# Kernel optimization log

Hardware: AMD Instinct MI355X
Metric: run time of the kernel (lower is better)

The kernel has to match this reference:

```python
import jax, jax.numpy as jnp
import numpy as np

N, E, A, S = 100000, 1600000, 500000, 50000
F_IN, W, LAYERS = 64, 64, 3


def setup_inputs() -> dict:
    key = jax.random.key(0)
    ks = jax.random.split(key, 20)

    def glorot(k, shape):
        fan_in = shape[-2]
        return jax.random.normal(k, shape, dtype=jnp.float32) / jnp.sqrt(jnp.float32(fan_in))

    return {
        "x": jax.random.normal(ks[0], (N, F_IN), dtype=jnp.float32),
        "edge_src": jax.random.randint(ks[1], (E,), 0, N, dtype=jnp.int32),
        "edge_dst": jax.random.randint(ks[2], (E,), 0, N, dtype=jnp.int32),
        "gather_idx": jax.random.randint(ks[3], (A,), 0, N, dtype=jnp.int32),
        "seg_idx": jax.random.randint(ks[4], (A,), 0, S, dtype=jnp.int32),
        # GraphConv 0: lin_root (no bias) + lin_rel (bias)
        "w_root0": glorot(ks[5], (F_IN, W)),
        "w_rel0": glorot(ks[6], (F_IN, W)),
        "b0": jnp.zeros((W,), jnp.float32),
        # hidden GraphConv layers, stacked
        "w_root_h": glorot(ks[7], (LAYERS - 1, W, W)),
        "w_rel_h": glorot(ks[8], (LAYERS - 1, W, W)),
        "b_h": jnp.zeros((LAYERS - 1, W), jnp.float32),
        # MLP head
        "fc1_w": glorot(ks[9], (W, W)),
        "fc1_b": jnp.zeros((W,), jnp.float32),
        "fc2_w": glorot(ks[10], (W, 32)),
        "fc2_b": jnp.zeros((32,), jnp.float32),
        "fc3_w": glorot(ks[11], (32, 2)),
        "fc3_b": jnp.zeros((2,), jnp.float32),
        "num_sets": S,
    }


def _graph_conv(h, edge_src, edge_dst, w_root, w_rel, b):
    # PyG GraphConv (aggr='add'): out_i = W_root h_i + W_rel * sum_{j->i} h_j + b
    agg = jax.ops.segment_sum(h[edge_src], edge_dst, num_segments=h.shape[0])
    return h @ w_root + agg @ w_rel + b


def reference(x, edge_src, edge_dst, gather_idx, seg_idx,
              w_root0, w_rel0, b0, w_root_h, w_rel_h, b_h,
              fc1_w, fc1_b, fc2_w, fc2_b, fc3_w, fc3_b, num_sets):
    h = jax.nn.elu(_graph_conv(x, edge_src, edge_dst, w_root0, w_rel0, b0))
    for i in range(w_root_h.shape[0]):
        h = jax.nn.elu(_graph_conv(h, edge_src, edge_dst, w_root_h[i], w_rel_h[i], b_h[i]))
    # set pooling: gather node rows then scatter_add into sets
    pooled = jax.ops.segment_sum(h[gather_idx], seg_idx, num_segments=num_sets)  # [S, W]
    h = jax.nn.elu(pooled @ fc1_w + fc1_b)
    # dropout p=0.5 is identity at inference
    h = jax.nn.elu(h @ fc2_w + fc2_b)
    logits = h @ fc3_w + fc3_b
    return jax.nn.log_softmax(logits, axis=1)
```

## Files before the change

### kernel.cpp

```cpp
#include <hip/hip_runtime.h>


#define FEAT 64
#define SH 9
#define BSZ 512
#define CH 512
#define CAP 12288
#define SCHUNK 1024
#define IDXE 256
#define HPAD 8
#define LCHUNK 3200

typedef unsigned short u16;
typedef __attribute__((ext_vector_type(8))) short bf16x8;
typedef __attribute__((ext_vector_type(4))) float f32x4;

__device__ __forceinline__ float bf2f(u16 u) {
  union { unsigned int i; float f; } c; c.i = ((unsigned int)u) << 16; return c.f;
}
__device__ __forceinline__ u16 f2bf(float f) {
  union { float f; unsigned int i; } c; c.f = f;
  unsigned int u = c.i;
  return (u16)((u + 0x7FFFu + ((u >> 16) & 1u)) >> 16);
}

__global__ void p1a2f_kernel(const int* __restrict__ kE, int* __restrict__ cE, int nE, int NBe,
                             const int* __restrict__ kP, int* __restrict__ cP, int nP, int NBp,
                             const float* __restrict__ x, u16* __restrict__ xb, int n4, int g_cvt,
                             const float* __restrict__ wr0, const float* __restrict__ wl0,
                             const float* __restrict__ wrh, const float* __restrict__ wlh,
                             u16* __restrict__ wpack) {
  __shared__ int hist[256];
  int tid = threadIdx.x, b = blockIdx.x;
  if (b < 2 * CH) {
    const int* keys; int* counts; int nK, NB, c;
    if (b < CH) { keys = kE; counts = cE; nK = nE; NB = NBe; c = b; }
    else        { keys = kP; counts = cP; nK = nP; NB = NBp; c = b - CH; }
    hist[tid] = 0;
    __syncthreads();
    int len = (nK + CH - 1) / CH;
    int cbeg = c * len, cend = min(nK, cbeg + len);
    for (int i = cbeg + tid; i < cend; i += 256) atomicAdd(&hist[keys[i] >> SH], 1);
    __syncthreads();
    if (tid < NB) counts[tid * CH + c] = hist[tid];
  } else if (b < 2 * CH + g_cvt) {
    int i = (b - 2 * CH) * 256 + tid;
    if (i < n4) {
      float4 v = ((const float4*)x)[i];
      ushort4 o = { f2bf(v.x), f2bf(v.y), f2bf(v.z), f2bf(v.w) };
      ((ushort4*)xb)[i] = o;
    }
  } else {
    int t4 = (b - 2 * CH - g_cvt) * 4 + (tid >> 6);
    if (t4 < 48) {
      int l = t4 >> 4, t = t4 & 15;
      int kt = t >> 2, nt = t & 3;
      int lane = tid & 63;
      const float* wr; const float* wl;
      if (l == 0) { wr = wr0; wl = wl0; }
      else        { wr = wrh + (l - 1) * FEAT * FEAT; wl = wlh + (l - 1) * FEAT * FEAT; }
      int n = nt * 16 + (lane & 15);
      int k0 = kt * 32 + (lane >> 4) * 8;
      u16* dst = wpack + (((size_t)l * 16 + t) * 64 + lane) * 8;
#pragma unroll
      for (int j = 0; j < 8; ++j) {
        int k = k0 + j;
        float v = (k < FEAT) ? wr[k * FEAT + n] : wl[(k - FEAT) * FEAT + n];
        dst[j] = f2bf(v);
      }
    }
  }
}

__global__ void scan1_kernel(int* __restrict__ d0, int* __restrict__ bs0, int L0, int nb0,
                             int* __restrict__ d1, int* __restrict__ bs1, int L1) {
  __shared__ int tsum[256];
  int tid = threadIdx.x, b = blockIdx.x;
  int* data; int* bsums; int L, c;
  if (b < nb0) { data = d0; bsums = bs0; L = L0; c = b; }
  else         { data = d1; bsums = bs1; L = L1; c = b - nb0; }
  int base = c * SCHUNK + tid * 4;
  int v[4];
#pragma unroll
  for (int i = 0; i < 4; ++i) v[i] = (base + i < L) ? data[base + i] : 0;
  int local = v[0] + v[1] + v[2] + v[3];
  tsum[tid] = local;
  __syncthreads();
  for (int off = 1; off < 256; off <<= 1) {
    int u = (tid >= off) ? tsum[tid - off] : 0;
    __syncthreads();
    tsum[tid] += u;
    __syncthreads();
  }
  int excl = tsum[tid] - local;
  if (tid == 255) bsums[c] = tsum[255];
  int run = excl;
#pragma unroll
  for (int i = 0; i < 4; ++i) {
    if (base + i < L) data[base + i] = run;
    run += v[i];
  }
}

__global__ void scan3_kernel(int* __restrict__ d0, const int* __restrict__ bs0,
                             int* __restrict__ bb0, int L0, int NB0, int tot0, int nb0, int g0,
                             int* __restrict__ d1, const int* __restrict__ bs1,
                             int* __restrict__ bb1, int L1, int NB1, int tot1, int nb1) {
  __shared__ int t[256];
  int b = blockIdx.x, tid = threadIdx.x;
  int* data; const int* bsums; int* bbase; int L, NB, tot, nb, i;
  if (b < g0) { data = d0; bsums = bs0; bbase = bb0; L = L0; NB = NB0; tot = tot0; nb = nb0; i = b * 256 + tid; }
  else        { data = d1; bsums = bs1; bbase = bb1; L = L1; NB = NB1; tot = tot1; nb = nb1; i = (b - g0) * 256 + tid; }
  int v = (tid < nb) ? bsums[tid] : 0;
  t[tid] = v;
  __syncthreads();
  for (int off = 1; off < 256; off <<= 1) {
    int u = (tid >= off) ? t[tid - off] : 0;
    __syncthreads();
    t[tid] += u;
    __syncthreads();
  }
  int incl = t[tid];
  __syncthreads();
  t[tid] = incl - v;
  __syncthreads();
  if (i < L) {
    int val = data[i] + t[i / SCHUNK];
    data[i] = val;
    if ((i & (CH - 1)) == 0) bbase[i / CH] = val;
  }
  if (i == 0) bbase[NB] = tot;
}

__global__ void __launch_bounds__(256)
p1b2_kernel(const int* __restrict__ s0, const int* __restrict__ k0,
            const int* __restrict__ c0, int* __restrict__ bin0, int n0, int NB0,
            const int* __restrict__ s1, const int* __restrict__ k1,
            const int* __restrict__ c1, int* __restrict__ bin1, int n1, int NB1) {
  __shared__ int s_bin[LCHUNK];
  __shared__ unsigned char s_bu[LCHUNK];
  __shared__ int lcur[256];
  __shared__ int gdiff[256];
  __shared__ int ts[256];
  int tid = threadIdx.x, b = blockIdx.x;
  const int* src; const int* keys; const int* counts; int* bin; int nE, NB, c;
  if (b < CH) { src = s0; keys = k0; counts = c0; bin = bin0; nE = n0; NB = NB0; c = b; }
  else        { src = s1; keys = k1; counts = c1; bin = bin1; nE = n1; NB = NB1; c = b - CH; }
  int len = (nE + CH - 1) / CH;
  int cbeg = c * len, cend = min(nE, cbeg + len);
  int L = cend - cbeg;

  int cur = 0, v = 0;
  if (tid < NB) {
    int f = tid * CH + c;
    cur = counts[f];
    int nxt = (f + 1 < NB * CH) ? counts[f + 1] : nE;
    v = nxt - cur;
  }
  ts[tid] = v;
  __syncthreads();
  for (int off = 1; off < 256; off <<= 1) {
    int u = (tid >= off) ? ts[tid - off] : 0;
    __syncthreads();
    ts[tid] += u;
    __syncthreads();
  }
  int excl = ts[tid] - v;
  lcur[tid] = excl;
  gdiff[tid] = cur - excl;
  __syncthreads();

  if (L <= LCHUNK) {
    for (int i = cbeg + tid; i < cend; i += 256) {
      int k = keys[i];
      int bu = k >> SH;
      int pos = atomicAdd(&lcur[bu], 1);
      s_bin[pos] = (src[i] << SH) | (k & (BSZ - 1));
      s_bu[pos] = (unsigned char)bu;
    }
    __syncthreads();
    for (int i = tid; i < L; i += 256) {
      int bu = s_bu[i];
      bin[gdiff[bu] + i] = s_bin[i];
    }
  } else {
    for (int i = cbeg + tid; i < cend; i += 256) {
      int k = keys[i];
      int bu = k >> SH;
      int pos = atomicAdd(&lcur[bu], 1);
      bin[gdiff[bu] + pos] = (src[i] << SH) | (k & (BSZ - 1));
    }
  }
}

__global__ void __launch_bounds__(256) p2_kernel(const int* __restrict__ bin0,
                                                 const int* __restrict__ bb0,
                                                 int* __restrict__ csr0, int* __restrict__ rs0,
                                                 int nn0, int NB0,
                                                 const int* __restrict__ bin1,
                                                 const int* __restrict__ bb1,
                                                 int* __restrict__ csr1, int* __restrict__ rs1,
                                                 int nn1) {
  __shared__ int s_csr[CAP];
  __shared__ int hist[BSZ];
  __shared__ int excl[BSZ];
  __shared__ int ts[256];
  int tid = threadIdx.x, bb = blockIdx.x;
  const int* bin; const int* bbase; int* csr; int* rs; int n_nodes, b;
  if (bb < NB0) { bin = bin0; bbase = bb0; csr = csr0; rs = rs0; n_nodes = nn0; b = bb; }
  else          { bin = bin1; bbase = bb1; csr = csr1; rs = rs1; n_nodes = nn1; b = bb - NB0; }
  int base = bbase[b];
  int cnt = bbase[b + 1] - base;
  int node_lo = b * BSZ;
  int nnode = min(BSZ, n_nodes - node_lo);

  hist[tid] = 0; hist[tid + 256] = 0;
  __syncthreads();
  for (int i = tid; i < cnt; i += 256) atomicAdd(&hist[bin[base + i] & (BSZ - 1)], 1);
  __syncthreads();

  int a0 = hist[2 * tid], a1 = hist[2 * tid + 1];
  int pair = a0 + a1;
  ts[tid] = pair;
  __syncthreads();
  for (int off = 1; off < 256; off <<= 1) {
    int u = (tid >= off) ? ts[tid - off] : 0;
    __syncthreads();
    ts[tid] += u;
    __syncthreads();
  }
  int pexcl = ts[tid] - pair;
  excl[2 * tid] = pexcl;
  excl[2 * tid + 1] = pexcl + a0;
  __syncthreads();

  for (int t = tid; t < nnode; t += 256) rs[node_lo + t] = base + excl[t];
  if (tid == 0 && node_lo + nnode >= n_nodes) rs[n_nodes] = bbase[(n_nodes + BSZ - 1) / BSZ];
  hist[tid] = excl[tid]; hist[tid + 256] = excl[tid + 256];
  __syncthreads();

  if (cnt <= CAP) {
    for (int i = tid; i < cnt; i += 256) {
      int e = bin[base + i];
      int pos = atomicAdd(&hist[e & (BSZ - 1)], 1);
      s_csr[pos] = e >> SH;
    }
    __syncthreads();
    for (int i = tid; i < cnt; i += 256) csr[base + i] = s_csr[i];
  } else {
    for (int i = tid; i < cnt; i += 256) {
      int e = bin[base + i];
      int pos = atomicAdd(&hist[e & (BSZ - 1)], 1);
      csr[base + pos] = e >> SH;
    }
  }
}

__device__ __forceinline__ float4 reduce_sub(float4 a) {
  a.x += __shfl_xor(a.x, 16, 64); a.y += __shfl_xor(a.y, 16, 64);
  a.z += __shfl_xor(a.z, 16, 64); a.w += __shfl_xor(a.w, 16, 64);
  a.x += __shfl_xor(a.x, 32, 64); a.y += __shfl_xor(a.y, 32, 64);
  a.z += __shfl_xor(a.z, 32, 64); a.w += __shfl_xor(a.w, 32, 64);
  return a;
}

__device__ __forceinline__ float4 wave_gather_acc(const u16* __restrict__ hb,
                                                  const int* idx,
                                                  int d, int sub, int ch) {
  float4 acc = {0.f, 0.f, 0.f, 0.f};
  int i = sub;
  for (; i + 12 < d; i += 16) {
    int s0 = idx[i], s1 = idx[i + 4], s2 = idx[i + 8], s3 = idx[i + 12];
    ushort4 a = ((const ushort4*)(hb + (size_t)s0 * FEAT))[ch];
    ushort4 b = ((const ushort4*)(hb + (size_t)s1 * FEAT))[ch];
    ushort4 c = ((const ushort4*)(hb + (size_t)s2 * FEAT))[ch];
    ushort4 e = ((const ushort4*)(hb + (size_t)s3 * FEAT))[ch];
    acc.x += (bf2f(a.x) + bf2f(b.x)) + (bf2f(c.x) + bf2f(e.x));
    acc.y += (bf2f(a.y) + bf2f(b.y)) + (bf2f(c.y) + bf2f(e.y));
    acc.z += (bf2f(a.z) + bf2f(b.z)) + (bf2f(c.z) + bf2f(e.z));
    acc.w += (bf2f(a.w) + bf2f(b.w)) + (bf2f(c.w) + bf2f(e.w));
  }
  for (; i + 4 < d; i += 8) {
    int s0 = idx[i], s1 = idx[i + 4];
    ushort4 a = ((const ushort4*)(hb + (size_t)s0 * FEAT))[ch];
    ushort4 b = ((const ushort4*)(hb + (size_t)s1 * FEAT))[ch];
    acc.x += bf2f(a.x) + bf2f(b.x);
    acc.y += bf2f(a.y) + bf2f(b.y);
    acc.z += bf2f(a.z) + bf2f(b.z);
    acc.w += bf2f(a.w) + bf2f(b.w);
  }
  if (i < d) {
    int s0 = idx[i];
    ushort4 a = ((const ushort4*)(hb + (size_t)s0 * FEAT))[ch];
    acc.x += bf2f(a.x); acc.y += bf2f(a.y);
    acc.z += bf2f(a.z); acc.w += bf2f(a.w);
  }
  return reduce_sub(acc);
}

__global__ void __launch_bounds__(512)
layer_fused_kernel(const u16* __restrict__ hb,
                   const int* __restrict__ rs,
                   const int* __restrict__ csr,
                   const u16* __restrict__ wpack,
                   const float* __restrict__ bias,
                   u16* __restrict__ outb, int n) {
  __shared__ u16 s_h[64][FEAT + HPAD];
  __shared__ u16 s_a[64][FEAT + HPAD];
  __shared__ int s_idx[8][IDXE];
  const int tid = threadIdx.x;
  const int wv = __builtin_amdgcn_readfirstlane(tid >> 6);
  const int lane = tid & 63;
  const int sub = lane >> 4;
  const int ch = lane & 15;
  const int base = blockIdx.x * 64;

  for (int it = 0; it < 2; ++it) {
    int idx = tid + it * 512;
    int nl = idx >> 4, c = idx & 15;
    int node = base + nl;
    if (node < n)
      *(ushort4*)&s_h[nl][c * 4] = ((const ushort4*)(hb + (size_t)node * FEAT))[c];
  }

  int wbase = base + wv * 8;
  if (wbase < n) {
    int r[9];
#pragma unroll
    for (int j = 0; j < 9; ++j) r[j] = rs[min(wbase + j, n)];
    int rbeg = r[0];
    int run = r[8] - rbeg;
    int* sidx = &s_idx[wv][0];
    bool staged = (run <= IDXE);
    if (staged) {
      for (int i = lane; i < run; i += 64) sidx[i] = csr[rbeg + i];
    }
    int nt = min(8, n - wbase);
    for (int t = 0; t < nt; ++t) {
      int d = r[t + 1] - r[t];
      float4 acc;
      if (staged) acc = wave_gather_acc(hb, sidx + (r[t] - rbeg), d, sub, ch);
      else        acc = wave_gather_acc(hb, csr + r[t], d, sub, ch);
      if (sub == 0) {
        ushort4 o = { f2bf(acc.x), f2bf(acc.y), f2bf(acc.z), f2bf(acc.w) };
        *(ushort4*)&s_a[wv * 8 + t][ch * 4] = o;
      }
    }
  }
  __syncthreads();

  const int mt = wv & 3;
  const int ntb = (wv >> 2) * 2;
  const int mrow = mt * 16 + (lane & 15);
  const int koff = (lane >> 4) * 8;
  f32x4 acc0 = {0.f, 0.f, 0.f, 0.f};
  f32x4 acc1 = {0.f, 0.f, 0.f, 0.f};
#pragma unroll
  for (int kt = 0; kt < 4; ++kt) {
    bf16x8 a;
    if (kt < 2) a = *(const bf16x8*)&s_h[mrow][kt * 32 + koff];
    else        a = *(const bf16x8*)&s_a[mrow][(kt - 2) * 32 + koff];
    bf16x8 b0 = *(const bf16x8*)&wpack[(((size_t)kt * 4 + ntb) * 64 + lane) * 8];
    bf16x8 b1 = *(const bf16x8*)&wpack[(((size_t)kt * 4 + ntb + 1) * 64 + lane) * 8];
    acc0 = __builtin_amdgcn_mfma_f32_16x16x32_bf16(a, b0, acc0, 0, 0, 0);
    acc1 = __builtin_amdgcn_mfma_f32_16x16x32_bf16(a, b1, acc1, 0, 0, 0);
  }
  __syncthreads();

  const int col = lane & 15;
  const int rbase = (lane >> 4) * 4;
  const float bs0 = bias[ntb * 16 + col];
  const float bs1 = bias[(ntb + 1) * 16 + col];
#pragma unroll
  for (int rg = 0; rg < 4; ++rg) {
    int nl = mt * 16 + rbase + rg;
    float v0 = acc0[rg] + bs0;
    float v1 = acc1[rg] + bs1;
    v0 = v0 > 0.f ? v0 : (__expf(v0) - 1.f);
    v1 = v1 > 0.f ? v1 : (__expf(v1) - 1.f);
    s_h[nl][ntb * 16 + col] = f2bf(v0);
    s_h[nl][(ntb + 1) * 16 + col] = f2bf(v1);
  }
  __syncthreads();

  for (int it = 0; it < 2; ++it) {
    int idx = tid + it * 512;
    int nl = idx >> 4, c = idx & 15;
    int node = base + nl;
    if (node < n)
      ((ushort4*)(outb + (size_t)node * FEAT))[c] = *(const ushort4*)&s_h[nl][c * 4];
  }
}

__global__ void __launch_bounds__(512)
pool_mlp_kernel(const u16* __restrict__ hb,
                const int* __restrict__ rs,
                const int* __restrict__ csr,
                const float* __restrict__ fc1_w, const float* __restrict__ fc1_b,
                const float* __restrict__ fc2_w, const float* __restrict__ fc2_b,
                const float* __restrict__ fc3_w, const float* __restrict__ fc3_b,
                float* __restrict__ out, int nsets) {
  __shared__ float s_p[64][FEAT + 4];
  __shared__ int s_idx[8][IDXE];
  const int tid = threadIdx.x;
  const int wv = __builtin_amdgcn_readfirstlane(tid >> 6);
  const int lane = tid & 63;
  const int sub = lane >> 4;
  const int ch = lane & 15;
  const int base = blockIdx.x * 64;

  int wbase = base + wv * 8;
  if (wbase < nsets) {
    int r[9];
#pragma unroll
    for (int j = 0; j < 9; ++j) r[j] = rs[min(wbase + j, nsets)];
    int rbeg = r[0];
    int run = r[8] - rbeg;
    int* sidx = &s_idx[wv][0];
    bool staged = (run <= IDXE);
    if (staged) {
      for (int i = lane; i < run; i += 64) sidx[i] = csr[rbeg + i];
    }
    int nt = min(8, nsets - wbase);
    for (int t = 0; t < nt; ++t) {
      int d = r[t + 1] - r[t];
      float4 acc;
      if (staged) acc = wave_gather_acc(hb, sidx + (r[t] - rbeg), d, sub, ch);
      else        acc = wave_gather_acc(hb, csr + r[t], d, sub, ch);
      if (sub == 0) *(float4*)&s_p[wv * 8 + t][ch * 4] = acc;
    }
  }
  __syncthreads();

  {
    const int jb = wv * 8;
    float acc[8];
#pragma unroll
    for (int jj = 0; jj < 8; ++jj) acc[jj] = fc1_b[jb + jj];
    for (int k = 0; k < FEAT; k += 4) {
      const float4 pv = *(const float4*)&s_p[lane][k];
      const float pk[4] = {pv.x, pv.y, pv.z, pv.w};
#pragma unroll
      for (int kk = 0; kk < 4; ++kk) {
        const float* w = fc1_w + (k + kk) * FEAT + jb;
#pragma unroll
        for (int jj = 0; jj < 8; ++jj) acc[jj] += pk[kk] * w[jj];
      }
    }
    __syncthreads();
#pragma unroll
    for (int jj = 0; jj < 8; ++jj) {
      float a = acc[jj];
      s_p[lane][jb + jj] = a > 0.f ? a : (__expf(a) - 1.f);
    }
  }
  __syncthreads();

  {
    const int jb = wv * 4;
    float acc[4];
#pragma unroll
    for (int jj = 0; jj < 4; ++jj) acc[jj] = fc2_b[jb + jj];
    for (int k = 0; k < FEAT; k += 4) {
      const float4 tv = *(const float4*)&s_p[lane][k];
      const float tk[4] = {tv.x, tv.y, tv.z, tv.w};
#pragma unroll
      for (int kk = 0; kk < 4; ++kk) {
        const float* w = fc2_w + (k + kk) * 32 + jb;
#pragma unroll
        for (int jj = 0; jj < 4; ++jj) acc[jj] += tk[kk] * w[jj];
      }
    }
    __syncthreads();
#pragma unroll
    for (int jj = 0; jj < 4; ++jj) {
      float a = acc[jj];
      s_p[lane][jb + jj] = a > 0.f ? a : (__expf(a) - 1.f);
    }
  }
  __syncthreads();

  if (wv == 0) {
    int s = base + lane;
    if (s < nsets) {
      float a0 = fc3_b[0], a1 = fc3_b[1];
      for (int k = 0; k < 32; k += 4) {
        const float4 tv = *(const float4*)&s_p[lane][k];
        const float tk[4] = {tv.x, tv.y, tv.z, tv.w};
#pragma unroll
        for (int kk = 0; kk < 4; ++kk) {
          a0 += tk[kk] * fc3_w[(k + kk) * 2 + 0];
          a1 += tk[kk] * fc3_w[(k + kk) * 2 + 1];
        }
      }
      float m = fmaxf(a0, a1);
      float lse = m + logf(__expf(a0 - m) + __expf(a1 - m));
      float2 r = {a0 - lse, a1 - lse};
      *(float2*)(out + (size_t)s * 2) = r;
    }
  }
}

extern "C" void kernel_launch(void* const* d_in, const int* in_sizes, int n_in,
                              void* d_out, int out_size, void* d_ws, size_t ws_size,
                              hipStream_t stream) {
  const float* x        = (const float*)d_in[0];
  const int* edge_src   = (const int*)d_in[1];
  const int* edge_dst   = (const int*)d_in[2];
  const int* gather_idx = (const int*)d_in[3];
  const int* seg_idx    = (const int*)d_in[4];
  const float* w_root0  = (const float*)d_in[5];
  const float* w_rel0   = (const float*)d_in[6];
  const float* b0       = (const float*)d_in[7];
  const float* w_root_h = (const float*)d_in[8];
  const float* w_rel_h  = (const float*)d_in[9];
  const float* b_h      = (const float*)d_in[10];
  const float* fc1_w    = (const float*)d_in[11];
  const float* fc1_b    = (const float*)d_in[12];
  const float* fc2_w    = (const float*)d_in[13];
  const float* fc2_b    = (const float*)d_in[14];
  const float* fc3_w    = (const float*)d_in[15];
  const float* fc3_b    = (const float*)d_in[16];

  const int N = in_sizes[0] / FEAT;
  const int E = in_sizes[1];
  const int A = in_sizes[3];
  const int S = out_size / 2;

  const int NB_e = (N + BSZ - 1) / BSZ;
  const int NB_p = (S + BSZ - 1) / BSZ;
  const int L_e = NB_e * CH, L_p = NB_p * CH;
  const int nb_e = (L_e + SCHUNK - 1) / SCHUNK;
  const int nb_p = (L_p + SCHUNK - 1) / SCHUNK;
  const int g_e = (L_e + 255) / 256, g_p = (L_p + 255) / 256;

  size_t hrow_bytes = (size_t)N * FEAT * sizeof(u16);
  char* ws = (char*)d_ws;
  size_t off = 0;
  auto alloc = [&](size_t bytes) { void* p = ws + off; off += (bytes + 15) & ~(size_t)15; return p; };
  u16* xb       = (u16*)alloc(hrow_bytes);
  u16* b1b      = (u16*)alloc(hrow_bytes);
  u16* b2b      = (u16*)alloc(hrow_bytes);
  int* csr_e    = (int*)alloc((size_t)E * 4);
  int* bin_e    = (int*)alloc((size_t)E * 4);
  int* rs_e     = (int*)alloc((size_t)(N + 1) * 4);
  int* counts_e = (int*)alloc((size_t)L_e * 4);
  int* bbase_e  = (int*)alloc((size_t)(NB_e + 1) * 4);
  int* csr_p    = (int*)alloc((size_t)A * 4);
  int* bin_p    = (int*)alloc((size_t)A * 4);
  int* rs_p     = (int*)alloc((size_t)(S + 1) * 4);
  int* counts_p = (int*)alloc((size_t)L_p * 4);
  int* bbase_p  = (int*)alloc((size_t)(NB_p + 1) * 4);
  int* bsums_e  = (int*)alloc(256 * 4);
  int* bsums_p  = (int*)alloc(256 * 4);
  u16* wpack    = (u16*)alloc((size_t)3 * 16 * 64 * 8 * sizeof(u16));

  dim3 blk(256);
  dim3 blk512(512);

  int n4 = N * FEAT / 4;
  int g_cvt = (n4 + 255) / 256;
  int g_pp = 12;

  p1a2f_kernel<<<2 * CH + g_cvt + g_pp, blk, 0, stream>>>(
      edge_dst, counts_e, E, NB_e, seg_idx, counts_p, A, NB_p,
      x, xb, n4, g_cvt, w_root0, w_rel0, w_root_h, w_rel_h, wpack);
  scan1_kernel<<<nb_e + nb_p, blk, 0, stream>>>(counts_e, bsums_e, L_e, nb_e,
                                                counts_p, bsums_p, L_p);
  scan3_kernel<<<g_e + g_p, blk, 0, stream>>>(counts_e, bsums_e, bbase_e, L_e, NB_e, E, nb_e, g_e,
                                              counts_p, bsums_p, bbase_p, L_p, NB_p, A, nb_p);
  p1b2_kernel<<<2 * CH, blk, 0, stream>>>(edge_src, edge_dst, counts_e, bin_e, E, NB_e,
                                          gather_idx, seg_idx, counts_p, bin_p, A, NB_p);
  p2_kernel<<<NB_e + NB_p, blk, 0, stream>>>(bin_e, bbase_e, csr_e, rs_e, N, NB_e,
                                             bin_p, bbase_p, csr_p, rs_p, S);

  int lgrid = (N + 63) / 64;
  int pgrid = (S + 63) / 64;

  layer_fused_kernel<<<lgrid, blk512, 0, stream>>>(xb, rs_e, csr_e, wpack,
                                                   b0, b1b, N);
  layer_fused_kernel<<<lgrid, blk512, 0, stream>>>(b1b, rs_e, csr_e, wpack + 16 * 64 * 8,
                                                   b_h, b2b, N);
  layer_fused_kernel<<<lgrid, blk512, 0, stream>>>(b2b, rs_e, csr_e, wpack + 2 * 16 * 64 * 8,
                                                   b_h + FEAT, b1b, N);

  pool_mlp_kernel<<<pgrid, blk512, 0, stream>>>(b1b, rs_p, csr_p,
                                                fc1_w, fc1_b, fc2_w, fc2_b, fc3_w, fc3_b,
                                                (float*)d_out, S);
}
```

Measured before the change: 296.6 us.

## Prefetch next node's neighbor rows and use zero sentinel row for branchless gathers

```diff
diff --git a/kernel.cpp b/kernel.cpp
--- a/kernel.cpp
+++ b/kernel.cpp
@@ -67,6 +67,13 @@
         int k = k0 + j;
         float v = (k < FEAT) ? wr[k * FEAT + n] : wl[(k - FEAT) * FEAT + n];
         dst[j] = f2bf(v);
+      }
+    } else if (t4 == 48) {
+      int lane = tid & 63;
+      if (lane < 16) {
+        int Nn = n4 >> 4;
+        ushort4 z = {0, 0, 0, 0};
+        ((ushort4*)(xb + (size_t)Nn * FEAT))[lane] = z;
       }
     }
   }
@@ -264,38 +271,75 @@
   return a;
 }
 
-__device__ __forceinline__ float4 wave_gather_acc(const u16* __restrict__ hb,
-                                                  const int* idx,
-                                                  int d, int sub, int ch) {
-  float4 acc = {0.f, 0.f, 0.f, 0.f};
-  int i = sub;
-  for (; i + 12 < d; i += 16) {
-    int s0 = idx[i], s1 = idx[i + 4], s2 = idx[i + 8], s3 = idx[i + 12];
-    ushort4 a = ((const ushort4*)(hb + (size_t)s0 * FEAT))[ch];
-    ushort4 b = ((const ushort4*)(hb + (size_t)s1 * FEAT))[ch];
-    ushort4 c = ((const ushort4*)(hb + (size_t)s2 * FEAT))[ch];
-    ushort4 e = ((const ushort4*)(hb + (size_t)s3 * FEAT))[ch];
-    acc.x += (bf2f(a.x) + bf2f(b.x)) + (bf2f(c.x) + bf2f(e.x));
-    acc.y += (bf2f(a.y) + bf2f(b.y)) + (bf2f(c.y) + bf2f(e.y));
-    acc.z += (bf2f(a.z) + bf2f(b.z)) + (bf2f(c.z) + bf2f(e.z));
-    acc.w += (bf2f(a.w) + bf2f(b.w)) + (bf2f(c.w) + bf2f(e.w));
-  }
-  for (; i + 4 < d; i += 8) {
-    int s0 = idx[i], s1 = idx[i + 4];
-    ushort4 a = ((const ushort4*)(hb + (size_t)s0 * FEAT))[ch];
-    ushort4 b = ((const ushort4*)(hb + (size_t)s1 * FEAT))[ch];
-    acc.x += bf2f(a.x) + bf2f(b.x);
-    acc.y += bf2f(a.y) + bf2f(b.y);
-    acc.z += bf2f(a.z) + bf2f(b.z);
-    acc.w += bf2f(a.w) + bf2f(b.w);
-  }
-  if (i < d) {
-    int s0 = idx[i];
-    ushort4 a = ((const ushort4*)(hb + (size_t)s0 * FEAT))[ch];
-    acc.x += bf2f(a.x); acc.y += bf2f(a.y);
-    acc.z += bf2f(a.z); acc.w += bf2f(a.w);
-  }
-  return reduce_sub(acc);
+struct RowB { ushort4 a, b, c, e; };
+
+__device__ __forceinline__ RowB load_b16(const u16* __restrict__ hb, const int* idx,
+                                         int i, int d, int ch, int sent) {
+  int j0 = idx[i], j1 = idx[i + 4], j2 = idx[i + 8], j3 = idx[i + 12];
+  j0 = (i      < d) ? j0 : sent;
+  j1 = (i + 4  < d) ? j1 : sent;
+  j2 = (i + 8  < d) ? j2 : sent;
+  j3 = (i + 12 < d) ? j3 : sent;
+  RowB r;
+  r.a = ((const ushort4*)(hb + (size_t)((unsigned)(j0 * FEAT))))[ch];
+  r.b = ((const ushort4*)(hb + (size_t)((unsigned)(j1 * FEAT))))[ch];
+  r.c = ((const ushort4*)(hb + (size_t)((unsigned)(j2 * FEAT))))[ch];
+  r.e = ((const ushort4*)(hb + (size_t)((unsigned)(j3 * FEAT))))[ch];
+  return r;
+}
+
+__device__ __forceinline__ float4 acc_b16(float4 acc, RowB r) {
+  acc.x += (bf2f(r.a.x) + bf2f(r.b.x)) + (bf2f(r.c.x) + bf2f(r.e.x));
+  acc.y += (bf2f(r.a.y) + bf2f(r.b.y)) + (bf2f(r.c.y) + bf2f(r.e.y));
+  acc.z += (bf2f(r.a.z) + bf2f(r.b.z)) + (bf2f(r.c.z) + bf2f(r.e.z));
+  acc.w += (bf2f(r.a.w) + bf2f(r.b.w)) + (bf2f(r.c.w) + bf2f(r.e.w));
+  return acc;
+}
+
+template <class FW>
+__device__ __forceinline__ void gather8(const u16* __restrict__ hb,
+                                        const int* __restrict__ rs,
+                                        const int* __restrict__ csr,
+                                        int* sidx, int wbase, int n, int sent,
+                                        int sub, int ch, int lane, FW&& wr) {
+  int r[9];
+#pragma unroll
+  for (int j = 0; j < 9; ++j) r[j] = rs[min(wbase + j, n)];
+  int rbeg = r[0];
+  int run = r[8] - rbeg;
+  const int* eb;
+  if (run <= IDXE) {
+    for (int i = lane; i < run; i += 64) sidx[i] = csr[rbeg + i];
+    eb = sidx;
+  } else {
+    eb = csr + rbeg;
+  }
+  int nt = min(8, n - wbase);
+  if (nt == 8) {
+    RowB cur = load_b16(hb, eb, sub, r[1] - r[0], ch, sent);
+#pragma unroll
+    for (int t = 0; t < 8; ++t) {
+      int off = r[t] - rbeg;
+      int d = r[t + 1] - r[t];
+      RowB nxt;
+      if (t < 7) nxt = load_b16(hb, eb + (r[t + 1] - rbeg), sub, r[t + 2] - r[t + 1], ch, sent);
+      float4 acc = {0.f, 0.f, 0.f, 0.f};
+      acc = acc_b16(acc, cur);
+      for (int i = sub + 16; i < d; i += 16)
+        acc = acc_b16(acc, load_b16(hb, eb + off, i, d, ch, sent));
+      wr(t, reduce_sub(acc));
+      if (t < 7) cur = nxt;
+    }
+  } else {
+    for (int t = 0; t < nt; ++t) {
+      int off = r[t] - rbeg;
+      int d = r[t + 1] - r[t];
+      float4 acc = {0.f, 0.f, 0.f, 0.f};
+      for (int i = sub; i < d; i += 16)
+        acc = acc_b16(acc, load_b16(hb, eb + off, i, d, ch, sent));
+      wr(t, reduce_sub(acc));
+    }
+  }
 }
 
 __global__ void __launch_bounds__(512)
@@ -307,7 +351,7 @@
                    u16* __restrict__ outb, int n) {
   __shared__ u16 s_h[64][FEAT + HPAD];
   __shared__ u16 s_a[64][FEAT + HPAD];
-  __shared__ int s_idx[8][IDXE];
+  __shared__ int s_idx[8][IDXE + 16];
   const int tid = threadIdx.x;
   const int wv = __builtin_amdgcn_readfirstlane(tid >> 6);
   const int lane = tid & 63;
@@ -325,27 +369,13 @@
 
   int wbase = base + wv * 8;
   if (wbase < n) {
-    int r[9];
-#pragma unroll
-    for (int j = 0; j < 9; ++j) r[j] = rs[min(wbase + j, n)];
-    int rbeg = r[0];
-    int run = r[8] - rbeg;
-    int* sidx = &s_idx[wv][0];
-    bool staged = (run <= IDXE);
-    if (staged) {
-      for (int i = lane; i < run; i += 64) sidx[i] = csr[rbeg + i];
-    }
-    int nt = min(8, n - wbase);
-    for (int t = 0; t < nt; ++t) {
-      int d = r[t + 1] - r[t];
-      float4 acc;
-      if (staged) acc = wave_gather_acc(hb, sidx + (r[t] - rbeg), d, sub, ch);
-      else        acc = wave_gather_acc(hb, csr + r[t], d, sub, ch);
-      if (sub == 0) {
-        ushort4 o = { f2bf(acc.x), f2bf(acc.y), f2bf(acc.z), f2bf(acc.w) };
-        *(ushort4*)&s_a[wv * 8 + t][ch * 4] = o;
-      }
-    }
+    gather8(hb, rs, csr, &s_idx[wv][0], wbase, n, n, sub, ch, lane,
+            [&](int t, float4 acc) {
+              if (sub == 0) {
+                ushort4 o = { f2bf(acc.x), f2bf(acc.y), f2bf(acc.z), f2bf(acc.w) };
+                *(ushort4*)&s_a[wv * 8 + t][ch * 4] = o;
+              }
+            });
   }
   __syncthreads();
 
@@ -390,6 +420,11 @@
     if (node < n)
       ((ushort4*)(outb + (size_t)node * FEAT))[c] = *(const ushort4*)&s_h[nl][c * 4];
   }
+
+  if (blockIdx.x == 0 && tid < 16) {
+    ushort4 z = {0, 0, 0, 0};
+    ((ushort4*)(outb + (size_t)n * FEAT))[tid] = z;
+  }
 }
 
 __global__ void __launch_bounds__(512)
@@ -399,9 +434,9 @@
                 const float* __restrict__ fc1_w, const float* __restrict__ fc1_b,
                 const float* __restrict__ fc2_w, const float* __restrict__ fc2_b,
                 const float* __restrict__ fc3_w, const float* __restrict__ fc3_b,
-                float* __restrict__ out, int nsets) {
+                float* __restrict__ out, int nsets, int nnodes) {
   __shared__ float s_p[64][FEAT + 4];
-  __shared__ int s_idx[8][IDXE];
+  __shared__ int s_idx[8][IDXE + 16];
   const int tid = threadIdx.x;
   const int wv = __builtin_amdgcn_readfirstlane(tid >> 6);
   const int lane = tid & 63;
@@ -411,24 +446,10 @@
 
   int wbase = base + wv * 8;
   if (wbase < nsets) {
-    int r[9];
-#pragma unroll
-    for (int j = 0; j < 9; ++j) r[j] = rs[min(wbase + j, nsets)];
-    int rbeg = r[0];
-    int run = r[8] - rbeg;
-    int* sidx = &s_idx[wv][0];
-    bool staged = (run <= IDXE);
-    if (staged) {
-      for (int i = lane; i < run; i += 64) sidx[i] = csr[rbeg + i];
-    }
-    int nt = min(8, nsets - wbase);
-    for (int t = 0; t < nt; ++t) {
-      int d = r[t + 1] - r[t];
-      float4 acc;
-      if (staged) acc = wave_gather_acc(hb, sidx + (r[t] - rbeg), d, sub, ch);
-      else        acc = wave_gather_acc(hb, csr + r[t], d, sub, ch);
-      if (sub == 0) *(float4*)&s_p[wv * 8 + t][ch * 4] = acc;
-    }
+    gather8(hb, rs, csr, &s_idx[wv][0], wbase, nsets, nnodes, sub, ch, lane,
+            [&](int t, float4 acc) {
+              if (sub == 0) *(float4*)&s_p[wv * 8 + t][ch * 4] = acc;
+            });
   }
   __syncthreads();
 
@@ -534,19 +555,19 @@
   const int nb_p = (L_p + SCHUNK - 1) / SCHUNK;
   const int g_e = (L_e + 255) / 256, g_p = (L_p + 255) / 256;
 
-  size_t hrow_bytes = (size_t)N * FEAT * sizeof(u16);
+  size_t hrow_bytes = (size_t)(N + 1) * FEAT * sizeof(u16);
   char* ws = (char*)d_ws;
   size_t off = 0;
   auto alloc = [&](size_t bytes) { void* p = ws + off; off += (bytes + 15) & ~(size_t)15; return p; };
   u16* xb       = (u16*)alloc(hrow_bytes);
   u16* b1b      = (u16*)alloc(hrow_bytes);
   u16* b2b      = (u16*)alloc(hrow_bytes);
-  int* csr_e    = (int*)alloc((size_t)E * 4);
+  int* csr_e    = (int*)alloc((size_t)(E + 16) * 4);
   int* bin_e    = (int*)alloc((size_t)E * 4);
   int* rs_e     = (int*)alloc((size_t)(N + 1) * 4);
   int* counts_e = (int*)alloc((size_t)L_e * 4);
   int* bbase_e  = (int*)alloc((size_t)(NB_e + 1) * 4);
-  int* csr_p    = (int*)alloc((size_t)A * 4);
+  int* csr_p    = (int*)alloc((size_t)(A + 16) * 4);
   int* bin_p    = (int*)alloc((size_t)A * 4);
   int* rs_p     = (int*)alloc((size_t)(S + 1) * 4);
   int* counts_p = (int*)alloc((size_t)L_p * 4);
@@ -560,7 +581,7 @@
 
   int n4 = N * FEAT / 4;
   int g_cvt = (n4 + 255) / 256;
-  int g_pp = 12;
+  int g_pp = 13;
 
   p1a2f_kernel<<<2 * CH + g_cvt + g_pp, blk, 0, stream>>>(
       edge_dst, counts_e, E, NB_e, seg_idx, counts_p, A, NB_p,
@@ -586,5 +607,5 @@
 
   pool_mlp_kernel<<<pgrid, blk512, 0, stream>>>(b1b, rs_p, csr_p,
                                                 fc1_w, fc1_b, fc2_w, fc2_b, fc3_w, fc3_b,
-                                                (float*)d_out, S);
-}
+                                                (float*)d_out, S, N);
+}
```

After: 288.1 us. 2.9% less time.
